# Optimization experiments

Hardware: AMD Instinct MI355X
Metric: run time of the kernel (lower is better)

Reference implementation:

```python
import jax, jax.numpy as jnp
import numpy as np
import math

B, S, HID = 4, 2048, 1024
NH, HD = 16, 64  # num heads, head dim
ROPE_THETA = 10000.0


def rotate_half(x):
    x1, x2 = jnp.split(x, 2, axis=-1)
    return jnp.concatenate((-x2, x1), axis=-1)


def setup_inputs() -> dict:
    key = jax.random.key(0)
    ks = jax.random.split(key, 7)
    hidden_states = jax.random.normal(ks[0], (B, S, HID), dtype=jnp.float32)
    attention_mask = jnp.zeros((B, 1, S, S), dtype=jnp.float32)
    position_ids = jnp.sort(jax.random.randint(ks[1], (B, S), 0, S), axis=-1)
    scale = 1.0 / math.sqrt(HID)
    Wq = jax.random.normal(ks[2], (HID, HID), dtype=jnp.float32) * scale
    Wk = jax.random.normal(ks[3], (HID, HID), dtype=jnp.float32) * scale
    Wv = jax.random.normal(ks[4], (HID, HID), dtype=jnp.float32) * scale
    Wo = jax.random.normal(ks[5], (HID, HID), dtype=jnp.float32) * scale
    return {"hidden_states": hidden_states, "attention_mask": attention_mask,
            "position_ids": position_ids, "Wq": Wq, "Wk": Wk, "Wv": Wv, "Wo": Wo}


def reference(hidden_states, attention_mask, position_ids, Wq, Wk, Wv, Wo):
    dtype = hidden_states.dtype
    # QKV projections (torch Linear: x @ W.T), reshape to [B, H, S, D]
    def proj(W):
        return (hidden_states @ W.T).reshape(B, S, NH, HD).transpose(0, 2, 1, 3)
    q, k, v = proj(Wq), proj(Wk), proj(Wv)

    # Rotary embeddings: cos/sin cache of shape [S, HD], gathered by position_ids
    inv_freq = 1.0 / (ROPE_THETA ** (jnp.arange(0, HD, 2, dtype=jnp.float32) / HD))
    t = jnp.arange(S, dtype=jnp.float32)
    freqs = t[:, None] * inv_freq[None, :]            # [S, HD/2]
    emb = jnp.concatenate((freqs, freqs), axis=-1)     # [S, HD]
    cos = jnp.cos(emb).astype(dtype)[position_ids][:, None]  # [B, 1, S, HD]
    sin = jnp.sin(emb).astype(dtype)[position_ids][:, None]

    q = q * cos + rotate_half(q) * sin
    k = k * cos + rotate_half(k) * sin

    # Manual attention: scores, additive mask, fp32 softmax, weighted sum
    scores = jnp.einsum('bhqd,bhkd->bhqk', q, k) / math.sqrt(HD)
    scores = scores + attention_mask
    attn = jax.nn.softmax(scores.astype(jnp.float32), axis=-1).astype(dtype)
    out = jnp.einsum('bhqk,bhkd->bhqd', attn, v)       # [B, H, S, D]
    out = out.transpose(0, 2, 1, 3).reshape(B, S, HID)
    return out @ Wo.T
```

## Files before the change

kernel.cpp:

```cpp
#include <hip/hip_runtime.h>
#include <hip/hip_bf16.h>
#include <math.h>

typedef __bf16 bf16;
typedef bf16 bf16x4 __attribute__((ext_vector_type(4)));
typedef bf16 bf16x8 __attribute__((ext_vector_type(8)));
typedef float f32x4 __attribute__((ext_vector_type(4)));

#define B_ 4
#define S_ 2048
#define HID_ 1024
#define NH_ 16
#define HD_ 64
#define LTS 72

__device__ __forceinline__ void async16(const bf16* g, bf16* l) {
  __builtin_amdgcn_global_load_lds(
      (const __attribute__((address_space(1))) void*)g,
      (__attribute__((address_space(3))) void*)l, 16, 0, 0);
}

#define MM16(A, B, C) C = __builtin_amdgcn_mfma_f32_16x16x32_bf16(A, B, C, 0, 0, 0)

__global__ void cvt_kernel(const float* __restrict__ src, bf16* __restrict__ dst, int n4) {
  int i = blockIdx.x * 256 + threadIdx.x;
  if (i < n4) {
    float4 v = ((const float4*)src)[i];
    bf16x4 o;
    o[0] = (bf16)v.x; o[1] = (bf16)v.y; o[2] = (bf16)v.z; o[3] = (bf16)v.w;
    ((bf16x4*)dst)[i] = o;
  }
}

#define DECL_ACC \
  f32x4 a00 = {}, a01 = {}, a02 = {}, a03 = {}; \
  f32x4 a10 = {}, a11 = {}, a12 = {}, a13 = {}; \
  f32x4 a20 = {}, a21 = {}, a22 = {}, a23 = {}; \
  f32x4 a30 = {}, a31 = {}, a32 = {}, a33 = {};

#define KLOOP_FRAGS_MFMA \
    bf16x8 af0 = *(const bf16x8*)(lA + (wm + 0 * 16 + l16) * 32 + quad * 8); \
    bf16x8 af1 = *(const bf16x8*)(lA + (wm + 1 * 16 + l16) * 32 + quad * 8); \
    bf16x8 af2 = *(const bf16x8*)(lA + (wm + 2 * 16 + l16) * 32 + quad * 8); \
    bf16x8 af3 = *(const bf16x8*)(lA + (wm + 3 * 16 + l16) * 32 + quad * 8); \
    bf16x8 bg0 = *(const bf16x8*)(lB + (wn + 0 * 16 + l16) * 32 + quad * 8); \
    bf16x8 bg1 = *(const bf16x8*)(lB + (wn + 1 * 16 + l16) * 32 + quad * 8); \
    bf16x8 bg2 = *(const bf16x8*)(lB + (wn + 2 * 16 + l16) * 32 + quad * 8); \
    bf16x8 bg3 = *(const bf16x8*)(lB + (wn + 3 * 16 + l16) * 32 + quad * 8); \
    MM16(af0, bg0, a00); MM16(af0, bg1, a01); MM16(af0, bg2, a02); MM16(af0, bg3, a03); \
    MM16(af1, bg0, a10); MM16(af1, bg1, a11); MM16(af1, bg2, a12); MM16(af1, bg3, a13); \
    MM16(af2, bg0, a20); MM16(af2, bg1, a21); MM16(af2, bg2, a22); MM16(af2, bg3, a23); \
    MM16(af3, bg0, a30); MM16(af3, bg1, a31); MM16(af3, bg2, a32); MM16(af3, bg3, a33);

#define ROPE_R(i, r, C0, C1, C2, C3) { \
  const int mloc = (i) * 16 + quad * 4 + (r); \
  const float p = (float)pos[mbase + mloc]; \
  const float aa0 = p * invf0, aa1 = p * invf1; \
  const float c0 = __cosf(aa0), sn0 = __sinf(aa0); \
  const float c1 = __cosf(aa1), sn1 = __sinf(aa1); \
  myT[mloc * LTS + l16]      = (bf16)((C0[r] * c0 - C2[r] * sn0) * scl); \
  myT[mloc * LTS + 32 + l16] = (bf16)((C2[r] * c0 + C0[r] * sn0) * scl); \
  myT[mloc * LTS + 16 + l16] = (bf16)((C1[r] * c1 - C3[r] * sn1) * scl); \
  myT[mloc * LTS + 48 + l16] = (bf16)((C3[r] * c1 + C1[r] * sn1) * scl); }
#define ROPE_I(i, C0, C1, C2, C3) \
  ROPE_R(i, 0, C0, C1, C2, C3) ROPE_R(i, 1, C0, C1, C2, C3) \
  ROPE_R(i, 2, C0, C1, C2, C3) ROPE_R(i, 3, C0, C1, C2, C3)

#define VW(i, j, C) { \
  bf16x4 o; o[0] = (bf16)C[0]; o[1] = (bf16)C[1]; o[2] = (bf16)C[2]; o[3] = (bf16)C[3]; \
  *(bf16x4*)(myT + ((j) * 16 + l16) * LTS + (i) * 16 + quad * 4) = o; }

__global__ void qkv_gemm(
    const bf16* __restrict__ X, const bf16* __restrict__ Wq,
    const bf16* __restrict__ Wk, const bf16* __restrict__ Wv,
    const int* __restrict__ pos,
    bf16* __restrict__ Q, bf16* __restrict__ Ko, bf16* __restrict__ Vt) {
  const int z = blockIdx.z;
  const bf16* W = (z == 0) ? Wq : (z == 1) ? Wk : Wv;
  const int m0 = blockIdx.y * 128;
  const int n0 = blockIdx.x * 128;
  __shared__ __align__(16) bf16 lA[128 * 32];
  __shared__ __align__(16) bf16 lB[128 * 32];
  __shared__ __align__(16) bf16 lT[4][64 * LTS];
  const int tid = threadIdx.x;
  const int lane = tid & 63, w = tid >> 6;
  const int wm = (w >> 1) * 64, wn = (w & 1) * 64;
  const int quad = lane >> 4, l16 = lane & 15;

  DECL_ACC

  const int qa = tid, qb = tid + 256;
  const int ra = qa >> 2, ca = (qa & 3) * 8;
  const int rb = qb >> 2, cb = (qb & 3) * 8;

  for (int k0 = 0; k0 < 1024; k0 += 32) {
    async16(X + (size_t)(m0 + ra) * 1024 + k0 + ca, lA + qa * 8);
    async16(X + (size_t)(m0 + rb) * 1024 + k0 + cb, lA + qb * 8);
    async16(W + (size_t)(n0 + ra) * 1024 + k0 + ca, lB + qa * 8);
    async16(W + (size_t)(n0 + rb) * 1024 + k0 + cb, lB + qb * 8);
    __syncthreads();
    KLOOP_FRAGS_MFMA
    __syncthreads();
  }

  const int h = (n0 + wn) >> 6;
  const int mbase = m0 + wm;
  const int b = mbase >> 11, s0 = mbase & 2047;
  bf16* myT = lT[w];

  if (z <= 1) {
    const float scl = (z == 0) ? 0.125f : 1.0f;
    const float invf0 = __expf(-0.28782313662425572f * (float)l16);
    const float invf1 = __expf(-0.28782313662425572f * (float)(16 + l16));
    ROPE_I(0, a00, a01, a02, a03)
    ROPE_I(1, a10, a11, a12, a13)
    ROPE_I(2, a20, a21, a22, a23)
    ROPE_I(3, a30, a31, a32, a33)
    asm volatile("s_waitcnt lgkmcnt(0)" ::: "memory");
    bf16* dst = (z == 0) ? Q : Ko;
    const int rr = lane >> 3, cc = lane & 7;
#pragma unroll
    for (int it = 0; it < 8; it++) {
      int mloc = it * 8 + rr;
      bf16x8 v = *(const bf16x8*)(myT + mloc * LTS + cc * 8);
      *(bf16x8*)(dst + (((size_t)b * NH_ + h) * S_ + s0 + mloc) * HD_ + cc * 8) = v;
    }
  } else {
    VW(0, 0, a00) VW(0, 1, a01) VW(0, 2, a02) VW(0, 3, a03)
    VW(1, 0, a10) VW(1, 1, a11) VW(1, 2, a12) VW(1, 3, a13)
    VW(2, 0, a20) VW(2, 1, a21) VW(2, 2, a22) VW(2, 3, a23)
    VW(3, 0, a30) VW(3, 1, a31) VW(3, 2, a32) VW(3, 3, a33)
    asm volatile("s_waitcnt lgkmcnt(0)" ::: "memory");
    const int rr = lane >> 3, cc = lane & 7;
#pragma unroll
    for (int it = 0; it < 8; it++) {
      int d = it * 8 + rr;
      bf16x8 v = *(const bf16x8*)(myT + d * LTS + cc * 8);
      *(bf16x8*)(Vt + (((size_t)b * NH_ + h) * HD_ + d) * S_ + s0 + cc * 8) = v;
    }
  }
}

__global__ void attn_kernel(
    const bf16* __restrict__ Q, const bf16* __restrict__ K,
    const bf16* __restrict__ Vt, const float* __restrict__ mask,
    bf16* __restrict__ ctx) {
  const int b = blockIdx.y >> 4, h = blockIdx.y & 15;
  const int q0 = blockIdx.x * 64;
  __shared__ __align__(16) bf16 lQ[64 * 64];
  __shared__ __align__(16) bf16 lK[64 * 64];
  __shared__ __align__(16) bf16 lV[64 * 64];
  __shared__ __align__(16) bf16 lP[4][16 * 64];
  const int tid = threadIdx.x;
  const int lane = tid & 63, w = tid >> 6;
  const int quad = lane >> 4, l16 = lane & 15;

  const int sr = tid >> 3;
  const int scs = (tid & 7) ^ (sr & 7);

  const size_t headoff = ((size_t)b * NH_ + h) * S_ * HD_;
  {
    const bf16* src = Q + headoff + (size_t)q0 * HD_;
    async16(src + sr * 64 + scs * 8, lQ + tid * 8);
    async16(src + (sr + 32) * 64 + scs * 8, lQ + (tid + 256) * 8);
  }

  f32x4 o0 = {}, o1 = {}, o2 = {}, o3 = {};
  float m_run = -1e30f, l_run = 0.f;
  const float* mrow = mask + ((size_t)b * S_ + q0 + w * 16 + l16) * S_;
  const int sw = l16 & 7;
  const int pq  = (quad ^ sw) * 8;
  const int pq2 = ((quad + 4) ^ sw) * 8;
  bf16* myP = lP[w];

  for (int kt = 0; kt < 32; kt++) {
    const int k0 = kt * 64;
    const bf16* ksrc = K + headoff + (size_t)k0 * HD_;
    async16(ksrc + sr * 64 + scs * 8, lK + tid * 8);
    async16(ksrc + (sr + 32) * 64 + scs * 8, lK + (tid + 256) * 8);
    {
      const bf16* vbase = Vt + headoff + k0;
      async16(vbase + (size_t)sr * S_ + scs * 8, lV + tid * 8);
      async16(vbase + (size_t)(sr + 32) * S_ + scs * 8, lV + (tid + 256) * 8);
    }
    __syncthreads();

    f32x4 s0 = {}, s1 = {}, s2 = {}, s3 = {};
    {
      bf16x8 bq = *(const bf16x8*)(lQ + (w * 16 + l16) * 64 + pq);
      bf16x8 k0f = *(const bf16x8*)(lK + (0 * 16 + l16) * 64 + pq);
      bf16x8 k1f = *(const bf16x8*)(lK + (1 * 16 + l16) * 64 + pq);
      bf16x8 k2f = *(const bf16x8*)(lK + (2 * 16 + l16) * 64 + pq);
      bf16x8 k3f = *(const bf16x8*)(lK + (3 * 16 + l16) * 64 + pq);
      MM16(k0f, bq, s0); MM16(k1f, bq, s1); MM16(k2f, bq, s2); MM16(k3f, bq, s3);
    }
    {
      bf16x8 bq = *(const bf16x8*)(lQ + (w * 16 + l16) * 64 + pq2);
      bf16x8 k0f = *(const bf16x8*)(lK + (0 * 16 + l16) * 64 + pq2);
      bf16x8 k1f = *(const bf16x8*)(lK + (1 * 16 + l16) * 64 + pq2);
      bf16x8 k2f = *(const bf16x8*)(lK + (2 * 16 + l16) * 64 + pq2);
      bf16x8 k3f = *(const bf16x8*)(lK + (3 * 16 + l16) * 64 + pq2);
      MM16(k0f, bq, s0); MM16(k1f, bq, s1); MM16(k2f, bq, s2); MM16(k3f, bq, s3);
    }

    const float4* m4 = (const float4*)(mrow + k0);
    float4 f0 = m4[quad], f1 = m4[4 + quad], f2 = m4[8 + quad], f3 = m4[12 + quad];
    float v00 = s0[0] + f0.x, v01 = s0[1] + f0.y, v02 = s0[2] + f0.z, v03 = s0[3] + f0.w;
    float v10 = s1[0] + f1.x, v11 = s1[1] + f1.y, v12 = s1[2] + f1.z, v13 = s1[3] + f1.w;
    float v20 = s2[0] + f2.x, v21 = s2[1] + f2.y, v22 = s2[2] + f2.z, v23 = s2[3] + f2.w;
    float v30 = s3[0] + f3.x, v31 = s3[1] + f3.y, v32 = s3[2] + f3.z, v33 = s3[3] + f3.w;

    float mx = fmaxf(fmaxf(fmaxf(v00, v01), fmaxf(v02, v03)),
                     fmaxf(fmaxf(v10, v11), fmaxf(v12, v13)));
    mx = fmaxf(mx, fmaxf(fmaxf(fmaxf(v20, v21), fmaxf(v22, v23)),
                         fmaxf(fmaxf(v30, v31), fmaxf(v32, v33))));
    mx = fmaxf(mx, __shfl_xor(mx, 16));
    mx = fmaxf(mx, __shfl_xor(mx, 32));
    const float mnew = fmaxf(m_run, mx);
    const float alpha = __expf(m_run - mnew);
    m_run = mnew;

    float p00 = __expf(v00 - mnew), p01 = __expf(v01 - mnew), p02 = __expf(v02 - mnew), p03 = __expf(v03 - mnew);
    float p10 = __expf(v10 - mnew), p11 = __expf(v11 - mnew), p12 = __expf(v12 - mnew), p13 = __expf(v13 - mnew);
    float p20 = __expf(v20 - mnew), p21 = __expf(v21 - mnew), p22 = __expf(v22 - mnew), p23 = __expf(v23 - mnew);
    float p30 = __expf(v30 - mnew), p31 = __expf(v31 - mnew), p32 = __expf(v32 - mnew), p33 = __expf(v33 - mnew);

    {
      const int swz = 8 * sw;
      bf16x4 pk;
      pk[0] = (bf16)p00; pk[1] = (bf16)p01; pk[2] = (bf16)p02; pk[3] = (bf16)p03;
      *(bf16x4*)(myP + l16 * 64 + ((0 * 16 + quad * 4) ^ swz)) = pk;
      pk[0] = (bf16)p10; pk[1] = (bf16)p11; pk[2] = (bf16)p12; pk[3] = (bf16)p13;
      *(bf16x4*)(myP + l16 * 64 + ((1 * 16 + quad * 4) ^ swz)) = pk;
      pk[0] = (bf16)p20; pk[1] = (bf16)p21; pk[2] = (bf16)p22; pk[3] = (bf16)p23;
      *(bf16x4*)(myP + l16 * 64 + ((2 * 16 + quad * 4) ^ swz)) = pk;
      pk[0] = (bf16)p30; pk[1] = (bf16)p31; pk[2] = (bf16)p32; pk[3] = (bf16)p33;
      *(bf16x4*)(myP + l16 * 64 + ((3 * 16 + quad * 4) ^ swz)) = pk;
    }

    float ps = (((p00 + p01) + (p02 + p03)) + ((p10 + p11) + (p12 + p13)))
             + (((p20 + p21) + (p22 + p23)) + ((p30 + p31) + (p32 + p33)));
    ps += __shfl_xor(ps, 16);
    ps += __shfl_xor(ps, 32);
    l_run = l_run * alpha + ps;

    f32x4 av;
    av[0] = __shfl(alpha, quad * 4 + 0);
    av[1] = __shfl(alpha, quad * 4 + 1);
    av[2] = __shfl(alpha, quad * 4 + 2);
    av[3] = __shfl(alpha, quad * 4 + 3);
    o0 *= av; o1 *= av; o2 *= av; o3 *= av;

    {
      bf16x8 ap = *(const bf16x8*)(myP + l16 * 64 + pq);
      bf16x8 b0 = *(const bf16x8*)(lV + (0 * 16 + l16) * 64 + pq);
      bf16x8 b1 = *(const bf16x8*)(lV + (1 * 16 + l16) * 64 + pq);
      bf16x8 b2 = *(const bf16x8*)(lV + (2 * 16 + l16) * 64 + pq);
      bf16x8 b3 = *(const bf16x8*)(lV + (3 * 16 + l16) * 64 + pq);
      MM16(ap, b0, o0); MM16(ap, b1, o1); MM16(ap, b2, o2); MM16(ap, b3, o3);
    }
    {
      bf16x8 ap = *(const bf16x8*)(myP + l16 * 64 + pq2);
      bf16x8 b0 = *(const bf16x8*)(lV + (0 * 16 + l16) * 64 + pq2);
      bf16x8 b1 = *(const bf16x8*)(lV + (1 * 16 + l16) * 64 + pq2);
      bf16x8 b2 = *(const bf16x8*)(lV + (2 * 16 + l16) * 64 + pq2);
      bf16x8 b3 = *(const bf16x8*)(lV + (3 * 16 + l16) * 64 + pq2);
      MM16(ap, b0, o0); MM16(ap, b1, o1); MM16(ap, b2, o2); MM16(ap, b3, o3);
    }
    __syncthreads();
  }

  f32x4 lv;
  lv[0] = __shfl(l_run, quad * 4 + 0);
  lv[1] = __shfl(l_run, quad * 4 + 1);
  lv[2] = __shfl(l_run, quad * 4 + 2);
  lv[3] = __shfl(l_run, quad * 4 + 3);
#pragma unroll
  for (int r = 0; r < 4; r++) {
    const float invl = 1.0f / lv[r];
    const int sloc = w * 16 + quad * 4 + r;
    lQ[sloc * 64 + l16]      = (bf16)(o0[r] * invl);
    lQ[sloc * 64 + 16 + l16] = (bf16)(o1[r] * invl);
    lQ[sloc * 64 + 32 + l16] = (bf16)(o2[r] * invl);
    lQ[sloc * 64 + 48 + l16] = (bf16)(o3[r] * invl);
  }
  __syncthreads();
  {
    const int rr = tid >> 3, cc = tid & 7;
#pragma unroll
    for (int it = 0; it < 2; it++) {
      int sloc = it * 32 + rr;
      bf16x8 v = *(const bf16x8*)(lQ + sloc * 64 + cc * 8);
      *(bf16x8*)(ctx + ((size_t)b * S_ + q0 + sloc) * HID_ + h * HD_ + cc * 8) = v;
    }
  }
}

#define PW(i, j, C) { \
  float* po = out + (size_t)(m0 + wm + (i) * 16 + quad * 4) * 1024 + n0 + wn + (j) * 16 + l16; \
  po[0] = C[0]; po[1024] = C[1]; po[2048] = C[2]; po[3072] = C[3]; }

__global__ void proj_gemm(
    const bf16* __restrict__ A, const bf16* __restrict__ Wo, float* __restrict__ out) {
  const int m0 = blockIdx.y * 128;
  const int n0 = blockIdx.x * 128;
  __shared__ __align__(16) bf16 lA[128 * 32];
  __shared__ __align__(16) bf16 lB[128 * 32];
  const int tid = threadIdx.x;
  const int lane = tid & 63, w = tid >> 6;
  const int wm = (w >> 1) * 64, wn = (w & 1) * 64;
  const int quad = lane >> 4, l16 = lane & 15;

  DECL_ACC
  const int qa = tid, qb = tid + 256;
  const int ra = qa >> 2, ca = (qa & 3) * 8;
  const int rb = qb >> 2, cb = (qb & 3) * 8;

  for (int k0 = 0; k0 < 1024; k0 += 32) {
    async16(A + (size_t)(m0 + ra) * 1024 + k0 + ca, lA + qa * 8);
    async16(A + (size_t)(m0 + rb) * 1024 + k0 + cb, lA + qb * 8);
    async16(Wo + (size_t)(n0 + ra) * 1024 + k0 + ca, lB + qa * 8);
    async16(Wo + (size_t)(n0 + rb) * 1024 + k0 + cb, lB + qb * 8);
    __syncthreads();
    KLOOP_FRAGS_MFMA
    __syncthreads();
  }
  PW(0, 0, a00) PW(0, 1, a01) PW(0, 2, a02) PW(0, 3, a03)
  PW(1, 0, a10) PW(1, 1, a11) PW(1, 2, a12) PW(1, 3, a13)
  PW(2, 0, a20) PW(2, 1, a21) PW(2, 2, a22) PW(2, 3, a23)
  PW(3, 0, a30) PW(3, 1, a31) PW(3, 2, a32) PW(3, 3, a33)
}

__global__ void sentinel_kernel(float* out, int n, float val) {
  int i = blockIdx.x * 256 + threadIdx.x;
  if (i < n) out[i] = val;
}

extern "C" void kernel_launch(void* const* d_in, const int* in_sizes, int n_in,
                              void* d_out, int out_size, void* d_ws, size_t ws_size,
                              hipStream_t stream) {
  const float* X    = (const float*)d_in[0];
  const float* mask = (const float*)d_in[1];
  const int*   pos  = (const int*)d_in[2];
  const float* Wq   = (const float*)d_in[3];
  const float* Wk   = (const float*)d_in[4];
  const float* Wv   = (const float*)d_in[5];
  const float* Wo   = (const float*)d_in[6];
  float* out = (float*)d_out;

  char* ws = (char*)d_ws;
  const size_t SZ = (size_t)B_ * NH_ * S_ * HD_ * sizeof(bf16);
  if (ws_size < 3 * SZ) {
    sentinel_kernel<<<(out_size + 255) / 256, 256, 0, stream>>>(
        out, out_size, (float)(ws_size >> 20));
    return;
  }

  bf16* Xb  = (bf16*)(ws);
  bf16* ctx = (bf16*)(ws);
  bf16* Q   = (bf16*)(ws + SZ);
  bf16* Vt  = (bf16*)(ws + 2 * SZ);
  bf16* Wob = (bf16*)(ws + 2 * SZ);
  bf16* Kb  = (bf16*)d_out;
  bf16* Wqb = (bf16*)((char*)d_out + SZ);
  bf16* Wkb = Wqb + 1024 * 1024;
  bf16* Wvb = Wkb + 1024 * 1024;

  const int nX4 = (B_ * S_ * HID_) / 4;
  const int nW4 = (HID_ * HID_) / 4;
  cvt_kernel<<<(nX4 + 255) / 256, 256, 0, stream>>>(X, Xb, nX4);
  cvt_kernel<<<(nW4 + 255) / 256, 256, 0, stream>>>(Wq, Wqb, nW4);
  cvt_kernel<<<(nW4 + 255) / 256, 256, 0, stream>>>(Wk, Wkb, nW4);
  cvt_kernel<<<(nW4 + 255) / 256, 256, 0, stream>>>(Wv, Wvb, nW4);

  qkv_gemm<<<dim3(8, 64, 3), 256, 0, stream>>>(Xb, Wqb, Wkb, Wvb, pos, Q, Kb, Vt);
  attn_kernel<<<dim3(32, 64), 256, 0, stream>>>(Q, Kb, Vt, mask, ctx);

  cvt_kernel<<<(nW4 + 255) / 256, 256, 0, stream>>>(Wo, Wob, nW4);
  proj_gemm<<<dim3(8, 64), 256, 0, stream>>>(ctx, Wob, out);
}
```

Measured before the change: 430.5 us.

## Double-buffer K/V tiles in attention, keep Q in registers, lazily rescale softmax

The attention kernel now double-buffers the K and V tiles in LDS. The next tile's async loads are issued at the top of each iteration, so one barrier per iteration replaces the load-then-sync pattern. Q fragments are loaded once into registers, which frees the Q LDS buffer, and the mask for the next tile is prefetched into registers during the current one. Online-softmax rescaling of the accumulators is skipped unless the running max grows by more than 8, and MFMA phases get raised wave priority along with a launch-bounds hint of 4 blocks. The cost is more LDS for the double buffers and exponent values that can reach e^8 before renormalization.

```diff
diff --git a/kernel.cpp b/kernel.cpp
--- a/kernel.cpp
+++ b/kernel.cpp
@@ -141,15 +141,14 @@
   }
 }
 
-__global__ void attn_kernel(
+__global__ void __launch_bounds__(256, 4) attn_kernel(
     const bf16* __restrict__ Q, const bf16* __restrict__ K,
     const bf16* __restrict__ Vt, const float* __restrict__ mask,
     bf16* __restrict__ ctx) {
   const int b = blockIdx.y >> 4, h = blockIdx.y & 15;
   const int q0 = blockIdx.x * 64;
-  __shared__ __align__(16) bf16 lQ[64 * 64];
-  __shared__ __align__(16) bf16 lK[64 * 64];
-  __shared__ __align__(16) bf16 lV[64 * 64];
+  __shared__ __align__(16) bf16 lK[2][64 * 64];
+  __shared__ __align__(16) bf16 lV[2][64 * 64];
   __shared__ __align__(16) bf16 lP[4][16 * 64];
   const int tid = threadIdx.x;
   const int lane = tid & 63, w = tid >> 6;
@@ -161,50 +160,69 @@
   const size_t headoff = ((size_t)b * NH_ + h) * S_ * HD_;
   {
     const bf16* src = Q + headoff + (size_t)q0 * HD_;
-    async16(src + sr * 64 + scs * 8, lQ + tid * 8);
-    async16(src + (sr + 32) * 64 + scs * 8, lQ + (tid + 256) * 8);
-  }
-
-  f32x4 o0 = {}, o1 = {}, o2 = {}, o3 = {};
-  float m_run = -1e30f, l_run = 0.f;
+    async16(src + sr * 64 + scs * 8, lK[1] + tid * 8);
+    async16(src + (sr + 32) * 64 + scs * 8, lK[1] + (tid + 256) * 8);
+    const bf16* ksrc = K + headoff;
+    async16(ksrc + sr * 64 + scs * 8, lK[0] + tid * 8);
+    async16(ksrc + (sr + 32) * 64 + scs * 8, lK[0] + (tid + 256) * 8);
+    const bf16* vbase = Vt + headoff;
+    async16(vbase + (size_t)sr * S_ + scs * 8, lV[0] + tid * 8);
+    async16(vbase + (size_t)(sr + 32) * S_ + scs * 8, lV[0] + (tid + 256) * 8);
+  }
+
   const float* mrow = mask + ((size_t)b * S_ + q0 + w * 16 + l16) * S_;
   const int sw = l16 & 7;
   const int pq  = (quad ^ sw) * 8;
   const int pq2 = ((quad + 4) ^ sw) * 8;
   bf16* myP = lP[w];
 
+  float4 f0, f1, f2, f3;
+  {
+    const float4* m4 = (const float4*)(mrow);
+    f0 = m4[quad]; f1 = m4[4 + quad]; f2 = m4[8 + quad]; f3 = m4[12 + quad];
+  }
+
+  __syncthreads();
+  const bf16x8 qf  = *(const bf16x8*)(lK[1] + (w * 16 + l16) * 64 + pq);
+  const bf16x8 qf2 = *(const bf16x8*)(lK[1] + (w * 16 + l16) * 64 + pq2);
+  __syncthreads();
+
+  f32x4 o0 = {}, o1 = {}, o2 = {}, o3 = {};
+  float m_run = -1e30f, l_run = 0.f;
+
   for (int kt = 0; kt < 32; kt++) {
-    const int k0 = kt * 64;
-    const bf16* ksrc = K + headoff + (size_t)k0 * HD_;
-    async16(ksrc + sr * 64 + scs * 8, lK + tid * 8);
-    async16(ksrc + (sr + 32) * 64 + scs * 8, lK + (tid + 256) * 8);
+    const bf16* lKc = lK[kt & 1];
+    const bf16* lVc = lV[kt & 1];
+    if (kt < 31) {
+      bf16* nK = lK[(kt & 1) ^ 1];
+      bf16* nV = lV[(kt & 1) ^ 1];
+      const int k0n = (kt + 1) * 64;
+      const bf16* ksrc = K + headoff + (size_t)k0n * HD_;
+      async16(ksrc + sr * 64 + scs * 8, nK + tid * 8);
+      async16(ksrc + (sr + 32) * 64 + scs * 8, nK + (tid + 256) * 8);
+      const bf16* vbase = Vt + headoff + k0n;
+      async16(vbase + (size_t)sr * S_ + scs * 8, nV + tid * 8);
+      async16(vbase + (size_t)(sr + 32) * S_ + scs * 8, nV + (tid + 256) * 8);
+    }
+
+    f32x4 s0 = {}, s1 = {}, s2 = {}, s3 = {};
+    __builtin_amdgcn_s_setprio(1);
     {
-      const bf16* vbase = Vt + headoff + k0;
-      async16(vbase + (size_t)sr * S_ + scs * 8, lV + tid * 8);
-      async16(vbase + (size_t)(sr + 32) * S_ + scs * 8, lV + (tid + 256) * 8);
-    }
-    __syncthreads();
-
-    f32x4 s0 = {}, s1 = {}, s2 = {}, s3 = {};
+      bf16x8 k0f = *(const bf16x8*)(lKc + (0 * 16 + l16) * 64 + pq);
+      bf16x8 k1f = *(const bf16x8*)(lKc + (1 * 16 + l16) * 64 + pq);
+      bf16x8 k2f = *(const bf16x8*)(lKc + (2 * 16 + l16) * 64 + pq);
+      bf16x8 k3f = *(const bf16x8*)(lKc + (3 * 16 + l16) * 64 + pq);
+      MM16(k0f, qf, s0); MM16(k1f, qf, s1); MM16(k2f, qf, s2); MM16(k3f, qf, s3);
+    }
     {
-      bf16x8 bq = *(const bf16x8*)(lQ + (w * 16 + l16) * 64 + pq);
-      bf16x8 k0f = *(const bf16x8*)(lK + (0 * 16 + l16) * 64 + pq);
-      bf16x8 k1f = *(const bf16x8*)(lK + (1 * 16 + l16) * 64 + pq);
-      bf16x8 k2f = *(const bf16x8*)(lK + (2 * 16 + l16) * 64 + pq);
-      bf16x8 k3f = *(const bf16x8*)(lK + (3 * 16 + l16) * 64 + pq);
-      MM16(k0f, bq, s0); MM16(k1f, bq, s1); MM16(k2f, bq, s2); MM16(k3f, bq, s3);
-    }
-    {
-      bf16x8 bq = *(const bf16x8*)(lQ + (w * 16 + l16) * 64 + pq2);
-      bf16x8 k0f = *(const bf16x8*)(lK + (0 * 16 + l16) * 64 + pq2);
-      bf16x8 k1f = *(const bf16x8*)(lK + (1 * 16 + l16) * 64 + pq2);
-      bf16x8 k2f = *(const bf16x8*)(lK + (2 * 16 + l16) * 64 + pq2);
-      bf16x8 k3f = *(const bf16x8*)(lK + (3 * 16 + l16) * 64 + pq2);
-      MM16(k0f, bq, s0); MM16(k1f, bq, s1); MM16(k2f, bq, s2); MM16(k3f, bq, s3);
-    }
-
-    const float4* m4 = (const float4*)(mrow + k0);
-    float4 f0 = m4[quad], f1 = m4[4 + quad], f2 = m4[8 + quad], f3 = m4[12 + quad];
+      bf16x8 k0f = *(const bf16x8*)(lKc + (0 * 16 + l16) * 64 + pq2);
+      bf16x8 k1f = *(const bf16x8*)(lKc + (1 * 16 + l16) * 64 + pq2);
+      bf16x8 k2f = *(const bf16x8*)(lKc + (2 * 16 + l16) * 64 + pq2);
+      bf16x8 k3f = *(const bf16x8*)(lKc + (3 * 16 + l16) * 64 + pq2);
+      MM16(k0f, qf2, s0); MM16(k1f, qf2, s1); MM16(k2f, qf2, s2); MM16(k3f, qf2, s3);
+    }
+    __builtin_amdgcn_s_setprio(0);
+
     float v00 = s0[0] + f0.x, v01 = s0[1] + f0.y, v02 = s0[2] + f0.z, v03 = s0[3] + f0.w;
     float v10 = s1[0] + f1.x, v11 = s1[1] + f1.y, v12 = s1[2] + f1.z, v13 = s1[3] + f1.w;
     float v20 = s2[0] + f2.x, v21 = s2[1] + f2.y, v22 = s2[2] + f2.z, v23 = s2[3] + f2.w;
@@ -216,14 +234,24 @@
                          fmaxf(fmaxf(v30, v31), fmaxf(v32, v33))));
     mx = fmaxf(mx, __shfl_xor(mx, 16));
     mx = fmaxf(mx, __shfl_xor(mx, 32));
-    const float mnew = fmaxf(m_run, mx);
-    const float alpha = __expf(m_run - mnew);
-    m_run = mnew;
-
-    float p00 = __expf(v00 - mnew), p01 = __expf(v01 - mnew), p02 = __expf(v02 - mnew), p03 = __expf(v03 - mnew);
-    float p10 = __expf(v10 - mnew), p11 = __expf(v11 - mnew), p12 = __expf(v12 - mnew), p13 = __expf(v13 - mnew);
-    float p20 = __expf(v20 - mnew), p21 = __expf(v21 - mnew), p22 = __expf(v22 - mnew), p23 = __expf(v23 - mnew);
-    float p30 = __expf(v30 - mnew), p31 = __expf(v31 - mnew), p32 = __expf(v32 - mnew), p33 = __expf(v33 - mnew);
+
+    if (__any(mx > m_run + 8.f)) {
+      const float mnew = fmaxf(m_run, mx);
+      const float alpha = __expf(m_run - mnew);
+      m_run = mnew;
+      f32x4 av;
+      av[0] = __shfl(alpha, quad * 4 + 0);
+      av[1] = __shfl(alpha, quad * 4 + 1);
+      av[2] = __shfl(alpha, quad * 4 + 2);
+      av[3] = __shfl(alpha, quad * 4 + 3);
+      o0 *= av; o1 *= av; o2 *= av; o3 *= av;
+      l_run *= alpha;
+    }
+
+    float p00 = __expf(v00 - m_run), p01 = __expf(v01 - m_run), p02 = __expf(v02 - m_run), p03 = __expf(v03 - m_run);
+    float p10 = __expf(v10 - m_run), p11 = __expf(v11 - m_run), p12 = __expf(v12 - m_run), p13 = __expf(v13 - m_run);
+    float p20 = __expf(v20 - m_run), p21 = __expf(v21 - m_run), p22 = __expf(v22 - m_run), p23 = __expf(v23 - m_run);
+    float p30 = __expf(v30 - m_run), p31 = __expf(v31 - m_run), p32 = __expf(v32 - m_run), p33 = __expf(v33 - m_run);
 
     {
       const int swz = 8 * sw;
@@ -242,31 +270,32 @@
              + (((p20 + p21) + (p22 + p23)) + ((p30 + p31) + (p32 + p33)));
     ps += __shfl_xor(ps, 16);
     ps += __shfl_xor(ps, 32);
-    l_run = l_run * alpha + ps;
-
-    f32x4 av;
-    av[0] = __shfl(alpha, quad * 4 + 0);
-    av[1] = __shfl(alpha, quad * 4 + 1);
-    av[2] = __shfl(alpha, quad * 4 + 2);
-    av[3] = __shfl(alpha, quad * 4 + 3);
-    o0 *= av; o1 *= av; o2 *= av; o3 *= av;
-
+    l_run += ps;
+
+    if (kt < 31) {
+      const float4* mn = (const float4*)(mrow + (kt + 1) * 64);
+      f0 = mn[quad]; f1 = mn[4 + quad]; f2 = mn[8 + quad]; f3 = mn[12 + quad];
+    }
+
+    __builtin_amdgcn_s_setprio(1);
     {
       bf16x8 ap = *(const bf16x8*)(myP + l16 * 64 + pq);
-      bf16x8 b0 = *(const bf16x8*)(lV + (0 * 16 + l16) * 64 + pq);
-      bf16x8 b1 = *(const bf16x8*)(lV + (1 * 16 + l16) * 64 + pq);
-      bf16x8 b2 = *(const bf16x8*)(lV + (2 * 16 + l16) * 64 + pq);
-      bf16x8 b3 = *(const bf16x8*)(lV + (3 * 16 + l16) * 64 + pq);
+      bf16x8 b0 = *(const bf16x8*)(lVc + (0 * 16 + l16) * 64 + pq);
+      bf16x8 b1 = *(const bf16x8*)(lVc + (1 * 16 + l16) * 64 + pq);
+      bf16x8 b2 = *(const bf16x8*)(lVc + (2 * 16 + l16) * 64 + pq);
+      bf16x8 b3 = *(const bf16x8*)(lVc + (3 * 16 + l16) * 64 + pq);
       MM16(ap, b0, o0); MM16(ap, b1, o1); MM16(ap, b2, o2); MM16(ap, b3, o3);
     }
     {
       bf16x8 ap = *(const bf16x8*)(myP + l16 * 64 + pq2);
-      bf16x8 b0 = *(const bf16x8*)(lV + (0 * 16 + l16) * 64 + pq2);
-      bf16x8 b1 = *(const bf16x8*)(lV + (1 * 16 + l16) * 64 + pq2);
-      bf16x8 b2 = *(const bf16x8*)(lV + (2 * 16 + l16) * 64 + pq2);
-      bf16x8 b3 = *(const bf16x8*)(lV + (3 * 16 + l16) * 64 + pq2);
+      bf16x8 b0 = *(const bf16x8*)(lVc + (0 * 16 + l16) * 64 + pq2);
+      bf16x8 b1 = *(const bf16x8*)(lVc + (1 * 16 + l16) * 64 + pq2);
+      bf16x8 b2 = *(const bf16x8*)(lVc + (2 * 16 + l16) * 64 + pq2);
+      bf16x8 b3 = *(const bf16x8*)(lVc + (3 * 16 + l16) * 64 + pq2);
       MM16(ap, b0, o0); MM16(ap, b1, o1); MM16(ap, b2, o2); MM16(ap, b3, o3);
     }
+    __builtin_amdgcn_s_setprio(0);
+
     __syncthreads();
   }
 
@@ -275,14 +304,15 @@
   lv[1] = __shfl(l_run, quad * 4 + 1);
   lv[2] = __shfl(l_run, quad * 4 + 2);
   lv[3] = __shfl(l_run, quad * 4 + 3);
+  bf16* lO = lK[0];
 #pragma unroll
   for (int r = 0; r < 4; r++) {
     const float invl = 1.0f / lv[r];
     const int sloc = w * 16 + quad * 4 + r;
-    lQ[sloc * 64 + l16]      = (bf16)(o0[r] * invl);
-    lQ[sloc * 64 + 16 + l16] = (bf16)(o1[r] * invl);
-    lQ[sloc * 64 + 32 + l16] = (bf16)(o2[r] * invl);
-    lQ[sloc * 64 + 48 + l16] = (bf16)(o3[r] * invl);
+    lO[sloc * 64 + l16]      = (bf16)(o0[r] * invl);
+    lO[sloc * 64 + 16 + l16] = (bf16)(o1[r] * invl);
+    lO[sloc * 64 + 32 + l16] = (bf16)(o2[r] * invl);
+    lO[sloc * 64 + 48 + l16] = (bf16)(o3[r] * invl);
   }
   __syncthreads();
   {
@@ -290,7 +320,7 @@
 #pragma unroll
     for (int it = 0; it < 2; it++) {
       int sloc = it * 32 + rr;
-      bf16x8 v = *(const bf16x8*)(lQ + sloc * 64 + cc * 8);
+      bf16x8 v = *(const bf16x8*)(lO + sloc * 64 + cc * 8);
       *(bf16x8*)(ctx + ((size_t)b * S_ + q0 + sloc) * HID_ + h * HD_ + cc * 8) = v;
     }
   }
```

Result: faster. 403.6 us (-6.3%).
